# Kernel tuning notes

Hardware: AMD Instinct MI355X
Metric: run time of the kernel (lower is better)

Reference implementation:

```python
import jax, jax.numpy as jnp
import numpy as np

T, B, D_IN, D_H = 1024, 128, 256, 256


def setup_inputs() -> dict:
    key = jax.random.key(0)
    ks = jax.random.split(key, 9)
    s_in = 1.0 / np.sqrt(D_IN + D_H)  # torch nn.Linear init scale
    inputs = jax.random.normal(ks[0], (T, B, D_IN), dtype=jnp.float32)
    def lin(kw, kb):
        W = jax.random.uniform(kw, (D_IN + D_H, D_H), jnp.float32, -s_in, s_in)
        b = jax.random.uniform(kb, (D_H,), jnp.float32, -s_in, s_in)
        return W, b
    Wf, bf = lin(ks[1], ks[2])
    Wi, bi = lin(ks[3], ks[4])
    Wg, bg = lin(ks[5], ks[6])
    Wo, bo = lin(ks[7], ks[8])
    return {"inputs": inputs, "Wf": Wf, "bf": bf, "Wi": Wi, "bi": bi,
            "Wg": Wg, "bg": bg, "Wo": Wo, "bo": bo}


def reference(inputs, Wf, bf, Wi, bi, Wg, bg, Wo, bo):
    Bsz = inputs.shape[1]
    h0 = jnp.zeros((Bsz, D_H), inputs.dtype)
    c0 = jnp.zeros((Bsz, D_H), inputs.dtype)

    def step(carry, x):
        hx, cx = carry
        combined = jnp.concatenate([x, hx], axis=1)  # [B, D_IN+D_H]
        f = jax.nn.sigmoid(combined @ Wf + bf)
        i = jax.nn.sigmoid(combined @ Wi + bi)
        g = jnp.tanh(combined @ Wg + bg)
        o = jax.nn.sigmoid(combined @ Wo + bo)
        cx = f * cx + i * g
        hx = o * jnp.tanh(cx)
        return (hx, cx), hx

    (hx, cx), outputs = jax.lax.scan(step, (h0, c0), inputs)
    return outputs, (hx, cx)
```

## Files before the change

kernel.cpp:

```cpp
#include <hip/hip_runtime.h>
#include <hip/hip_bf16.h>

typedef short s16x8 __attribute__((ext_vector_type(8)));
typedef int   i32x4 __attribute__((ext_vector_type(4)));
typedef unsigned u32x2 __attribute__((ext_vector_type(2)));
typedef float f32x4 __attribute__((ext_vector_type(4)));
typedef float f32x2 __attribute__((ext_vector_type(2)));

#define T_STEPS 1024
#define BATCH   128
#define DIN     256
#define DH      256
#define NWG     64
#define NTHREADS 256

static __device__ __forceinline__ short f2bf(float f){ return __builtin_bit_cast(short,(__bf16)f); }
static __device__ __forceinline__ float sigf(float x){ return 1.f/(1.f+__expf(-x)); }
static __device__ __forceinline__ float tanhfast(float x){ return 1.f-2.f/(1.f+__expf(2.f*x)); }

static __device__ __forceinline__ i32x4 ld16_cc(const void* p){
  i32x4 r; asm volatile("global_load_dwordx4 %0, %1, off sc0 sc1" : "=v"(r) : "v"(p) : "memory"); return r;
}
static __device__ __forceinline__ unsigned ld4_cc(const void* p){
  unsigned r; asm volatile("global_load_dword %0, %1, off sc0 sc1\ns_waitcnt vmcnt(0)" : "=v"(r) : "v"(p) : "memory"); return r;
}
static __device__ __forceinline__ void st4_cc(void* p, unsigned v){
  asm volatile("global_store_dword %0, %1, off sc0 sc1" :: "v"(p), "v"(v) : "memory");
}
static __device__ __forceinline__ void st8t_cc(void* p, u32x2 v){
  asm volatile("global_store_dwordx2 %0, %1, off sc0 sc1" :: "v"(p), "v"(v) : "memory");
}
static __device__ __forceinline__ void st8_p(void* p, f32x2 v){
  asm volatile("global_store_dwordx2 %0, %1, off" :: "v"(p), "v"(v) : "memory");
}

static __device__ __forceinline__ s16x8 cvt8(f32x4 a, f32x4 b){
  s16x8 r;
  r[0]=f2bf(a[0]); r[1]=f2bf(a[1]); r[2]=f2bf(a[2]); r[3]=f2bf(a[3]);
  r[4]=f2bf(b[0]); r[5]=f2bf(b[1]); r[6]=f2bf(b[2]); r[7]=f2bf(b[3]);
  return r;
}

__global__ __launch_bounds__(NTHREADS, 1)
void lstm_v11(const float* __restrict__ X,
              const float* __restrict__ Wf, const float* __restrict__ bfv,
              const float* __restrict__ Wi, const float* __restrict__ biv,
              const float* __restrict__ Wg, const float* __restrict__ bgv,
              const float* __restrict__ Wo, const float* __restrict__ bov,
              float* __restrict__ out,
              unsigned* __restrict__ htag,
              unsigned* __restrict__ flags)
{
  const int bid = blockIdx.x;
  const int g   = bid & 7;
  const int csl = bid >> 3;
  const int tid = threadIdx.x;
  const int lane = tid & 63, wv = tid >> 6;
  const int grp = lane >> 4, l15 = lane & 15;
  const int r0 = g * 16;

  __shared__ short a_lds[2 * 32 * 16 * 8];
  __shared__ float elds[16 * 132];

  s16x8 bfr[2][16];
  {
    const float* Wm[4] = {Wf, Wi, Wg, Wo};
    const int gate = l15 >> 2, jj = l15 & 3;
    const float* Wsrc = Wm[gate];
#pragma unroll
    for (int n2 = 0; n2 < 2; ++n2) {
      const int hc = csl * 32 + (wv * 2 + n2) * 4 + jj;
#pragma unroll
      for (int kk = 0; kk < 16; ++kk) {
        const float* p = Wsrc + (size_t)(kk * 32 + grp * 8) * DH + hc;
        s16x8 f;
#pragma unroll
        for (int s = 0; s < 8; ++s) f[s] = f2bf(p[(size_t)s * DH]);
        bfr[n2][kk] = f;
      }
    }
  }

  const int erow = tid >> 4;
  const int j2   = tid & 15;
  const int ntl  = j2 >> 1;
  const int jjl  = (j2 & 1) * 2;
  float bia[4][2];
  {
    const float* Bv[4] = {bfv, biv, bgv, bov};
#pragma unroll
    for (int q = 0; q < 4; ++q) {
      bia[q][0] = Bv[q][csl * 32 + 2 * j2];
      bia[q][1] = Bv[q][csl * 32 + 2 * j2 + 1];
    }
  }

  const int xrow = tid & 15, xseg = tid >> 4;
  f32x4 xp0, xp1, xp2, xp3;
  {
    const float* xs = X + (size_t)(r0 + xrow) * DIN + xseg * 16;
    s16x8 lo = cvt8(*(const f32x4*)xs, *(const f32x4*)(xs + 4));
    s16x8 hi = cvt8(*(const f32x4*)(xs + 8), *(const f32x4*)(xs + 12));
    *(s16x8*)&a_lds[((2 * xseg + 0) * 16 + xrow) * 8] = lo;
    *(s16x8*)&a_lds[((2 * xseg + 1) * 16 + xrow) * 8] = hi;
    const float* xn = X + ((size_t)1 * BATCH + r0 + xrow) * DIN + xseg * 16;
    xp0 = *(const f32x4*)xn;       xp1 = *(const f32x4*)(xn + 4);
    xp2 = *(const f32x4*)(xn + 8); xp3 = *(const f32x4*)(xn + 12);
  }
  __syncthreads();

  unsigned* myflag = flags + (g * 32 + csl);
  const unsigned* pollp = flags + (g * 32 + (lane & 7));
  float cs0 = 0.f, cs1 = 0.f, h0s = 0.f, h1s = 0.f;

  for (int t = 0; t < T_STEPS; ++t) {
    const unsigned tte = (unsigned)t << 16;

    while (1) {
      unsigned v = ld4_cc(pollp);
      if (__all((int)(v >= (unsigned)t))) break;
    }
    __builtin_amdgcn_sched_barrier(0);

    const unsigned* hb = htag + (size_t)(t & 1) * (BATCH * DH)
                       + (size_t)(r0 + l15) * DH + grp * 8;
    i32x4 hraw[16];
#pragma unroll
    for (int q = 0; q < 8; ++q) {
      hraw[2 * q]     = ld16_cc(hb + q * 32);
      hraw[2 * q + 1] = ld16_cc(hb + q * 32 + 4);
    }

    {
      short* ab = a_lds + ((t + 1) & 1) * (32 * 16 * 8);
      s16x8 lo = cvt8(xp0, xp1), hi = cvt8(xp2, xp3);
      *(s16x8*)&ab[((2 * xseg + 0) * 16 + xrow) * 8] = lo;
      *(s16x8*)&ab[((2 * xseg + 1) * 16 + xrow) * 8] = hi;
    }

    const short* ar = a_lds + (t & 1) * (32 * 16 * 8);
    f32x4 acc0 = {0.f,0.f,0.f,0.f}, acc1 = {0.f,0.f,0.f,0.f};
#pragma unroll
    for (int kk = 0; kk < 8; ++kk) {
      s16x8 a = *(const s16x8*)&ar[((kk * 4 + grp) * 16 + l15) * 8];
      acc0 = __builtin_amdgcn_mfma_f32_16x16x32_bf16(a, bfr[0][kk], acc0, 0, 0, 0);
      acc1 = __builtin_amdgcn_mfma_f32_16x16x32_bf16(a, bfr[1][kk], acc1, 0, 0, 0);
    }

    asm volatile("s_waitcnt vmcnt(0)" ::: "memory");
    __builtin_amdgcn_sched_barrier(0);
    {
      int guardo = 1 << 16;
      while (1) {
        unsigned bad = 0;
#pragma unroll
        for (int i = 0; i < 16; ++i)
          bad |= (unsigned)(hraw[i][0] ^ (int)tte) | (unsigned)(hraw[i][1] ^ (int)tte)
               | (unsigned)(hraw[i][2] ^ (int)tte) | (unsigned)(hraw[i][3] ^ (int)tte);
        bad &= 0xFFFF0000u;
        if (__all((int)(bad == 0))) break;
        if (--guardo < 0) break;
#pragma unroll
        for (int q = 0; q < 8; ++q) {
          hraw[2 * q]     = ld16_cc(hb + q * 32);
          hraw[2 * q + 1] = ld16_cc(hb + q * 32 + 4);
        }
        asm volatile("s_waitcnt vmcnt(0)" ::: "memory");
        __builtin_amdgcn_sched_barrier(0);
      }
    }

#pragma unroll
    for (int q = 0; q < 8; ++q) {
      i32x4 hp;
      hp[0] = (int)__builtin_amdgcn_perm((unsigned)hraw[2*q][1],   (unsigned)hraw[2*q][0],   0x05040100u);
      hp[1] = (int)__builtin_amdgcn_perm((unsigned)hraw[2*q][3],   (unsigned)hraw[2*q][2],   0x05040100u);
      hp[2] = (int)__builtin_amdgcn_perm((unsigned)hraw[2*q+1][1], (unsigned)hraw[2*q+1][0], 0x05040100u);
      hp[3] = (int)__builtin_amdgcn_perm((unsigned)hraw[2*q+1][3], (unsigned)hraw[2*q+1][2], 0x05040100u);
      s16x8 ah = __builtin_bit_cast(s16x8, hp);
      acc0 = __builtin_amdgcn_mfma_f32_16x16x32_bf16(ah, bfr[0][8 + q], acc0, 0, 0, 0);
      acc1 = __builtin_amdgcn_mfma_f32_16x16x32_bf16(ah, bfr[1][8 + q], acc1, 0, 0, 0);
    }

#pragma unroll
    for (int rr = 0; rr < 4; ++rr) {
      elds[(grp * 4 + rr) * 132 + (wv * 2 + 0) * 16 + l15] = acc0[rr];
      elds[(grp * 4 + rr) * 132 + (wv * 2 + 1) * 16 + l15] = acc1[rr];
    }
    asm volatile("s_waitcnt lgkmcnt(0)" ::: "memory");
    __builtin_amdgcn_sched_barrier(0);
    __builtin_amdgcn_s_barrier();
    __builtin_amdgcn_sched_barrier(0);

    const float* ez = &elds[erow * 132 + ntl * 16];
    float h0, h1;
    {
      float zf = ez[0 + jjl] + bia[0][0], zi = ez[4 + jjl] + bia[1][0];
      float zg = ez[8 + jjl] + bia[2][0], zo = ez[12 + jjl] + bia[3][0];
      float cn = sigf(zf) * cs0 + sigf(zi) * tanhfast(zg);
      h0 = sigf(zo) * tanhfast(cn); cs0 = cn; h0s = h0;
    }
    {
      float zf = ez[1 + jjl] + bia[0][1], zi = ez[5 + jjl] + bia[1][1];
      float zg = ez[9 + jjl] + bia[2][1], zo = ez[13 + jjl] + bia[3][1];
      float cn = sigf(zf) * cs1 + sigf(zi) * tanhfast(zg);
      h1 = sigf(zo) * tanhfast(cn); cs1 = cn; h1s = h1;
    }

    const int rowg = r0 + erow;
    {
      const unsigned ttw = (unsigned)(t + 1) << 16;
      u32x2 hp2;
      hp2[0] = (unsigned)(unsigned short)f2bf(h0) | ttw;
      hp2[1] = (unsigned)(unsigned short)f2bf(h1) | ttw;
      st8t_cc(htag + (size_t)((t + 1) & 1) * (BATCH * DH)
              + (size_t)rowg * DH + csl * 32 + 2 * j2, hp2);
    }
    __builtin_amdgcn_sched_barrier(0);
    __builtin_amdgcn_s_barrier();
    __builtin_amdgcn_sched_barrier(0);
    if (tid == 0) st4_cc(myflag, (unsigned)(t + 1));

    {
      f32x2 ov; ov[0] = h0; ov[1] = h1;
      st8_p(out + ((size_t)t * BATCH + rowg) * DH + csl * 32 + 2 * j2, ov);
    }
    {
      const int tp = (t + 2 < T_STEPS) ? t + 2 : T_STEPS - 1;
      const float* xs = X + ((size_t)tp * BATCH + r0 + xrow) * DIN + xseg * 16;
      xp0 = *(const f32x4*)xs;       xp1 = *(const f32x4*)(xs + 4);
      xp2 = *(const f32x4*)(xs + 8); xp3 = *(const f32x4*)(xs + 12);
    }
  }

  {
    const size_t base = (size_t)T_STEPS * BATCH * DH;
    const size_t idx  = (size_t)(r0 + erow) * DH + csl * 32 + 2 * j2;
    out[base + idx]     = h0s;
    out[base + idx + 1] = h1s;
    out[base + BATCH * DH + idx]     = cs0;
    out[base + BATCH * DH + idx + 1] = cs1;
  }
}

__global__ __launch_bounds__(NTHREADS, 1)
void lstm_v10_fb(const float* __restrict__ X,
                 const float* __restrict__ Wf, const float* __restrict__ bfv,
                 const float* __restrict__ Wi, const float* __restrict__ biv,
                 const float* __restrict__ Wg, const float* __restrict__ bgv,
                 const float* __restrict__ Wo, const float* __restrict__ bov,
                 float* __restrict__ out,
                 unsigned short* __restrict__ hbuf,
                 unsigned int* __restrict__ flags)
{
  const int bid = blockIdx.x;
  const int g   = bid & 7;
  const int csl = bid >> 3;
  const int tid = threadIdx.x;
  const int lane = tid & 63, wv = tid >> 6;
  const int grp = lane >> 4, l15 = lane & 15;
  const int r0 = g * 16;

  __shared__ short a_lds[2 * 32 * 16 * 8];
  __shared__ float elds[4 * 16 * 36];

  s16x8 bfr[2][16];
  {
    const float* Wm[4] = {Wf, Wi, Wg, Wo};
    const int gate = l15 >> 2, jj = l15 & 3;
    const float* Wsrc = Wm[gate];
#pragma unroll
    for (int n2 = 0; n2 < 2; ++n2) {
      const int hc = csl * 32 + (wv * 2 + n2) * 4 + jj;
#pragma unroll
      for (int kk = 0; kk < 16; ++kk) {
        const float* p = Wsrc + (size_t)(kk * 32 + grp * 8) * DH + hc;
        s16x8 f;
#pragma unroll
        for (int s = 0; s < 8; ++s) f[s] = f2bf(p[(size_t)s * DH]);
        bfr[n2][kk] = f;
      }
    }
  }
  const int colg = csl * 32 + wv * 8 + 2 * grp;
  float bia[4][2];
  {
    const float* Bv[4] = {bfv, biv, bgv, bov};
#pragma unroll
    for (int q = 0; q < 4; ++q) { bia[q][0] = Bv[q][colg]; bia[q][1] = Bv[q][colg + 1]; }
  }
  const int xrow = tid & 15, xseg = tid >> 4;
  f32x4 xp0, xp1, xp2, xp3;
  {
    const float* xs = X + (size_t)(r0 + xrow) * DIN + xseg * 16;
    s16x8 lo = cvt8(*(const f32x4*)xs, *(const f32x4*)(xs + 4));
    s16x8 hi = cvt8(*(const f32x4*)(xs + 8), *(const f32x4*)(xs + 12));
    *(s16x8*)&a_lds[((2 * xseg + 0) * 16 + xrow) * 8] = lo;
    *(s16x8*)&a_lds[((2 * xseg + 1) * 16 + xrow) * 8] = hi;
    const float* xn = X + ((size_t)1 * BATCH + r0 + xrow) * DIN + xseg * 16;
    xp0 = *(const f32x4*)xn;       xp1 = *(const f32x4*)(xn + 4);
    xp2 = *(const f32x4*)(xn + 8); xp3 = *(const f32x4*)(xn + 12);
  }
  __syncthreads();

  unsigned* myflag = flags + (g * 32 + csl * 4 + wv);
  const unsigned* pollp = flags + (g * 32 + (lane & 31));
  float* eldsw = &elds[wv * 16 * 36];
  float cs0 = 0.f, cs1 = 0.f, h0s = 0.f, h1s = 0.f;

  for (int t = 0; t < T_STEPS; ++t) {
    while (1) {
      unsigned v = ld4_cc(pollp);
      if (__all((int)(v >= (unsigned)t))) break;
    }
    __builtin_amdgcn_sched_barrier(0);
    const unsigned short* hr = hbuf + (size_t)(t & 1) * (BATCH * DH)
                             + (size_t)(r0 + l15) * DH + grp * 8;
    i32x4 hraw[8];
#pragma unroll
    for (int q = 0; q < 8; ++q) hraw[q] = ld16_cc(hr + q * 32);
    {
      short* ab = a_lds + ((t + 1) & 1) * (32 * 16 * 8);
      s16x8 lo = cvt8(xp0, xp1), hi = cvt8(xp2, xp3);
      *(s16x8*)&ab[((2 * xseg + 0) * 16 + xrow) * 8] = lo;
      *(s16x8*)&ab[((2 * xseg + 1) * 16 + xrow) * 8] = hi;
    }
    const short* ar = a_lds + (t & 1) * (32 * 16 * 8);
    f32x4 acc0 = {0.f,0.f,0.f,0.f}, acc1 = {0.f,0.f,0.f,0.f};
#pragma unroll
    for (int kk = 0; kk < 8; ++kk) {
      s16x8 a = *(const s16x8*)&ar[((kk * 4 + grp) * 16 + l15) * 8];
      acc0 = __builtin_amdgcn_mfma_f32_16x16x32_bf16(a, bfr[0][kk], acc0, 0, 0, 0);
      acc1 = __builtin_amdgcn_mfma_f32_16x16x32_bf16(a, bfr[1][kk], acc1, 0, 0, 0);
    }
    asm volatile("s_waitcnt vmcnt(0)" ::: "memory");
    __builtin_amdgcn_sched_barrier(0);
#pragma unroll
    for (int q = 0; q < 8; ++q) {
      s16x8 ah = __builtin_bit_cast(s16x8, hraw[q]);
      acc0 = __builtin_amdgcn_mfma_f32_16x16x32_bf16(ah, bfr[0][8 + q], acc0, 0, 0, 0);
      acc1 = __builtin_amdgcn_mfma_f32_16x16x32_bf16(ah, bfr[1][8 + q], acc1, 0, 0, 0);
    }
#pragma unroll
    for (int rr = 0; rr < 4; ++rr) {
      eldsw[(grp * 4 + rr) * 36 + l15]      = acc0[rr];
      eldsw[(grp * 4 + rr) * 36 + 16 + l15] = acc1[rr];
    }
    asm volatile("s_waitcnt lgkmcnt(0)" ::: "memory");
    __builtin_amdgcn_sched_barrier(0);
    float z0[4], z1[4];
    const int hc0 = 2 * grp, hc1 = 2 * grp + 1;
#pragma unroll
    for (int q = 0; q < 4; ++q) {
      z0[q] = eldsw[l15 * 36 + ((hc0 >> 2) << 4) + 4 * q + (hc0 & 3)];
      z1[q] = eldsw[l15 * 36 + ((hc1 >> 2) << 4) + 4 * q + (hc1 & 3)];
    }
    {
      float zf = z0[0] + bia[0][0], zi = z0[1] + bia[1][0];
      float zg = z0[2] + bia[2][0], zo = z0[3] + bia[3][0];
      cs0 = sigf(zf) * cs0 + sigf(zi) * tanhfast(zg);
      h0s = sigf(zo) * tanhfast(cs0);
    }
    {
      float zf = z1[0] + bia[0][1], zi = z1[1] + bia[1][1];
      float zg = z1[2] + bia[2][1], zo = z1[3] + bia[3][1];
      cs1 = sigf(zf) * cs1 + sigf(zi) * tanhfast(zg);
      h1s = sigf(zo) * tanhfast(cs1);
    }
    const int row = r0 + l15;
    {
      unsigned hpk = (unsigned)(unsigned short)f2bf(h0s)
                   | ((unsigned)(unsigned short)f2bf(h1s) << 16);
      st4_cc(hbuf + (size_t)((t + 1) & 1) * (BATCH * DH)
             + (size_t)row * DH + colg, hpk);
      f32x2 ov; ov[0] = h0s; ov[1] = h1s;
      st8_p(out + ((size_t)t * BATCH + row) * DH + colg, ov);
    }
    asm volatile("s_waitcnt vmcnt(1)" ::: "memory");
    if (lane == 0) st4_cc(myflag, (unsigned)(t + 1));
    {
      const int tp = (t + 2 < T_STEPS) ? t + 2 : T_STEPS - 1;
      const float* xs = X + ((size_t)tp * BATCH + r0 + xrow) * DIN + xseg * 16;
      xp0 = *(const f32x4*)xs;       xp1 = *(const f32x4*)(xs + 4);
      xp2 = *(const f32x4*)(xs + 8); xp3 = *(const f32x4*)(xs + 12);
    }
  }
  {
    const unsigned* fp = flags + tid;
    while (ld4_cc(fp) < (unsigned)T_STEPS) __builtin_amdgcn_s_sleep(1);
    __syncthreads();
  }
  {
    const size_t base = (size_t)T_STEPS * BATCH * DH;
    const size_t idx  = (size_t)(r0 + l15) * DH + colg;
    out[base + idx]     = h0s;
    out[base + idx + 1] = h1s;
    out[base + BATCH * DH + idx]     = cs0;
    out[base + BATCH * DH + idx + 1] = cs1;
  }
}

extern "C" void kernel_launch(void* const* d_in, const int* in_sizes, int n_in,
                              void* d_out, int out_size, void* d_ws, size_t ws_size,
                              hipStream_t stream) {
  const float* X   = (const float*)d_in[0];
  const float* Wf  = (const float*)d_in[1];
  const float* bf_ = (const float*)d_in[2];
  const float* Wi  = (const float*)d_in[3];
  const float* bi_ = (const float*)d_in[4];
  const float* Wg  = (const float*)d_in[5];
  const float* bg_ = (const float*)d_in[6];
  const float* Wo  = (const float*)d_in[7];
  const float* bo_ = (const float*)d_in[8];
  float* out = (float*)d_out;

  const size_t tagbytes = (size_t)2 * BATCH * DH * 4;
  const size_t fbytes   = 1024;
  if (ws_size >= tagbytes + fbytes) {
    unsigned* htag  = (unsigned*)d_ws;
    unsigned* flags = (unsigned*)((unsigned char*)d_ws + tagbytes);
    hipMemsetAsync(d_ws, 0, tagbytes + fbytes, stream);
    lstm_v11<<<NWG, NTHREADS, 0, stream>>>(X, Wf, bf_, Wi, bi_, Wg, bg_,
                                           Wo, bo_, out, htag, flags);
    return;
  }
  unsigned char* tail = (unsigned char*)d_out + (size_t)T_STEPS * BATCH * DH * 4;
  unsigned short* hbuf = (unsigned short*)tail;
  unsigned int* flags  = (unsigned int*)(tail + 131072);
  hipMemsetAsync(tail, 0, 131072 + 1024, stream);
  lstm_v10_fb<<<NWG, NTHREADS, 0, stream>>>(X, Wf, bf_, Wi, bi_, Wg, bg_,
                                            Wo, bo_, out, hbuf, flags);
}
```

Measured before the change: 3.761 ms.

## Replace per-step flag barrier with polling on step-tagged hidden-state words

The main kernel drops the per-workgroup step flags, the workgroup barrier and the flag store after each step. Consumers now poll a sample of the tagged hidden-state words (a 16-bit step tag packed next to the bf16 value) until every tag matches the current step, then load the full slice and check it again. This takes the barrier and flag round trip off the critical path of the 1024-step recurrence. In exchange each step issues extra spin loads, and correctness now relies only on the per-word tags, with guard counters that break out of the spin loops.

```diff
diff --git a/kernel.cpp b/kernel.cpp
--- a/kernel.cpp
+++ b/kernel.cpp
@@ -21,6 +21,9 @@
 static __device__ __forceinline__ i32x4 ld16_cc(const void* p){
   i32x4 r; asm volatile("global_load_dwordx4 %0, %1, off sc0 sc1" : "=v"(r) : "v"(p) : "memory"); return r;
 }
+static __device__ __forceinline__ unsigned ld4i_cc(const void* p){
+  unsigned r; asm volatile("global_load_dword %0, %1, off sc0 sc1" : "=v"(r) : "v"(p) : "memory"); return r;
+}
 static __device__ __forceinline__ unsigned ld4_cc(const void* p){
   unsigned r; asm volatile("global_load_dword %0, %1, off sc0 sc1\ns_waitcnt vmcnt(0)" : "=v"(r) : "v"(p) : "memory"); return r;
 }
@@ -33,6 +36,8 @@
 static __device__ __forceinline__ void st8_p(void* p, f32x2 v){
   asm volatile("global_store_dwordx2 %0, %1, off" :: "v"(p), "v"(v) : "memory");
 }
+#define VM0 do { asm volatile("s_waitcnt vmcnt(0)" ::: "memory"); \
+  __builtin_amdgcn_sched_barrier(0); } while (0)
 
 static __device__ __forceinline__ s16x8 cvt8(f32x4 a, f32x4 b){
   s16x8 r;
@@ -42,14 +47,13 @@
 }
 
 __global__ __launch_bounds__(NTHREADS, 1)
-void lstm_v11(const float* __restrict__ X,
+void lstm_v12(const float* __restrict__ X,
               const float* __restrict__ Wf, const float* __restrict__ bfv,
               const float* __restrict__ Wi, const float* __restrict__ biv,
               const float* __restrict__ Wg, const float* __restrict__ bgv,
               const float* __restrict__ Wo, const float* __restrict__ bov,
               float* __restrict__ out,
-              unsigned* __restrict__ htag,
-              unsigned* __restrict__ flags)
+              unsigned* __restrict__ htag)
 {
   const int bid = blockIdx.x;
   const int g   = bid & 7;
@@ -109,21 +113,29 @@
   }
   __syncthreads();
 
-  unsigned* myflag = flags + (g * 32 + csl);
-  const unsigned* pollp = flags + (g * 32 + (lane & 7));
   float cs0 = 0.f, cs1 = 0.f, h0s = 0.f, h1s = 0.f;
 
   for (int t = 0; t < T_STEPS; ++t) {
     const unsigned tte = (unsigned)t << 16;
-
-    while (1) {
-      unsigned v = ld4_cc(pollp);
-      if (__all((int)(v >= (unsigned)t))) break;
-    }
-    __builtin_amdgcn_sched_barrier(0);
-
     const unsigned* hb = htag + (size_t)(t & 1) * (BATCH * DH)
                        + (size_t)(r0 + l15) * DH + grp * 8;
+
+    {
+      int guard = 1 << 16;
+      while (1) {
+        unsigned s[8];
+#pragma unroll
+        for (int q = 0; q < 8; ++q) s[q] = ld4i_cc(hb + q * 32);
+        VM0;
+        unsigned bad = 0;
+#pragma unroll
+        for (int q = 0; q < 8; ++q) bad |= (s[q] ^ tte);
+        bad &= 0xFFFF0000u;
+        if (__all((int)(bad == 0))) break;
+        if (--guard < 0) break;
+      }
+    }
+
     i32x4 hraw[16];
 #pragma unroll
     for (int q = 0; q < 8; ++q) {
@@ -147,10 +159,9 @@
       acc1 = __builtin_amdgcn_mfma_f32_16x16x32_bf16(a, bfr[1][kk], acc1, 0, 0, 0);
     }
 
-    asm volatile("s_waitcnt vmcnt(0)" ::: "memory");
-    __builtin_amdgcn_sched_barrier(0);
-    {
-      int guardo = 1 << 16;
+    VM0;
+    {
+      int guard = 1 << 14;
       while (1) {
         unsigned bad = 0;
 #pragma unroll
@@ -159,14 +170,13 @@
                | (unsigned)(hraw[i][2] ^ (int)tte) | (unsigned)(hraw[i][3] ^ (int)tte);
         bad &= 0xFFFF0000u;
         if (__all((int)(bad == 0))) break;
-        if (--guardo < 0) break;
+        if (--guard < 0) break;
 #pragma unroll
         for (int q = 0; q < 8; ++q) {
           hraw[2 * q]     = ld16_cc(hb + q * 32);
           hraw[2 * q + 1] = ld16_cc(hb + q * 32 + 4);
         }
-        asm volatile("s_waitcnt vmcnt(0)" ::: "memory");
-        __builtin_amdgcn_sched_barrier(0);
+        VM0;
       }
     }
 
@@ -216,10 +226,6 @@
       st8t_cc(htag + (size_t)((t + 1) & 1) * (BATCH * DH)
               + (size_t)rowg * DH + csl * 32 + 2 * j2, hp2);
     }
-    __builtin_amdgcn_sched_barrier(0);
-    __builtin_amdgcn_s_barrier();
-    __builtin_amdgcn_sched_barrier(0);
-    if (tid == 0) st4_cc(myflag, (unsigned)(t + 1));
 
     {
       f32x2 ov; ov[0] = h0; ov[1] = h1;
@@ -243,15 +249,18 @@
   }
 }
 
+static __device__ __forceinline__ i32x4 ld16f_cc(const void* p){
+  i32x4 r; asm volatile("global_load_dwordx4 %0, %1, off sc0 sc1" : "=v"(r) : "v"(p) : "memory"); return r;
+}
 __global__ __launch_bounds__(NTHREADS, 1)
-void lstm_v10_fb(const float* __restrict__ X,
-                 const float* __restrict__ Wf, const float* __restrict__ bfv,
-                 const float* __restrict__ Wi, const float* __restrict__ biv,
-                 const float* __restrict__ Wg, const float* __restrict__ bgv,
-                 const float* __restrict__ Wo, const float* __restrict__ bov,
-                 float* __restrict__ out,
-                 unsigned short* __restrict__ hbuf,
-                 unsigned int* __restrict__ flags)
+void lstm_fb(const float* __restrict__ X,
+             const float* __restrict__ Wf, const float* __restrict__ bfv,
+             const float* __restrict__ Wi, const float* __restrict__ biv,
+             const float* __restrict__ Wg, const float* __restrict__ bgv,
+             const float* __restrict__ Wo, const float* __restrict__ bov,
+             float* __restrict__ out,
+             unsigned short* __restrict__ hbuf,
+             unsigned int* __restrict__ flags)
 {
   const int bid = blockIdx.x;
   const int g   = bid & 7;
@@ -318,7 +327,7 @@
                              + (size_t)(r0 + l15) * DH + grp * 8;
     i32x4 hraw[8];
 #pragma unroll
-    for (int q = 0; q < 8; ++q) hraw[q] = ld16_cc(hr + q * 32);
+    for (int q = 0; q < 8; ++q) hraw[q] = ld16f_cc(hr + q * 32);
     {
       short* ab = a_lds + ((t + 1) & 1) * (32 * 16 * 8);
       s16x8 lo = cvt8(xp0, xp1), hi = cvt8(xp2, xp3);
@@ -333,8 +342,7 @@
       acc0 = __builtin_amdgcn_mfma_f32_16x16x32_bf16(a, bfr[0][kk], acc0, 0, 0, 0);
       acc1 = __builtin_amdgcn_mfma_f32_16x16x32_bf16(a, bfr[1][kk], acc1, 0, 0, 0);
     }
-    asm volatile("s_waitcnt vmcnt(0)" ::: "memory");
-    __builtin_amdgcn_sched_barrier(0);
+    VM0;
 #pragma unroll
     for (int q = 0; q < 8; ++q) {
       s16x8 ah = __builtin_bit_cast(s16x8, hraw[q]);
@@ -415,19 +423,17 @@
   float* out = (float*)d_out;
 
   const size_t tagbytes = (size_t)2 * BATCH * DH * 4;
-  const size_t fbytes   = 1024;
-  if (ws_size >= tagbytes + fbytes) {
-    unsigned* htag  = (unsigned*)d_ws;
-    unsigned* flags = (unsigned*)((unsigned char*)d_ws + tagbytes);
-    hipMemsetAsync(d_ws, 0, tagbytes + fbytes, stream);
-    lstm_v11<<<NWG, NTHREADS, 0, stream>>>(X, Wf, bf_, Wi, bi_, Wg, bg_,
-                                           Wo, bo_, out, htag, flags);
+  if (ws_size >= tagbytes) {
+    unsigned* htag = (unsigned*)d_ws;
+    hipMemsetAsync(d_ws, 0, tagbytes, stream);
+    lstm_v12<<<NWG, NTHREADS, 0, stream>>>(X, Wf, bf_, Wi, bi_, Wg, bg_,
+                                           Wo, bo_, out, htag);
     return;
   }
   unsigned char* tail = (unsigned char*)d_out + (size_t)T_STEPS * BATCH * DH * 4;
   unsigned short* hbuf = (unsigned short*)tail;
   unsigned int* flags  = (unsigned int*)(tail + 131072);
   hipMemsetAsync(tail, 0, 131072 + 1024, stream);
-  lstm_v10_fb<<<NWG, NTHREADS, 0, stream>>>(X, Wf, bf_, Wi, bi_, Wg, bg_,
-                                            Wo, bo_, out, hbuf, flags);
-}
+  lstm_fb<<<NWG, NTHREADS, 0, stream>>>(X, Wf, bf_, Wi, bi_, Wg, bg_,
+                                        Wo, bo_, out, hbuf, flags);
+}
```

Result: slower. 4.631 ms (+23.1%).
